# Kernel optimization log

Hardware: AMD Instinct MI355X
Metric: run time of the kernel (lower is better)

## Reference

```python
import jax, jax.numpy as jnp
import numpy as np
from jax.scipy.special import erfc

CUTOFF = 10.0   # real-space cutoff (Angstrom)
ALPHA = 0.3     # Ewald splitting parameter (1/Angstrom)
KMAX = 8        # max integer k-index per dimension
N_ATOMS = 4096
BOX = 40.0      # cubic box edge (Angstrom)


def setup_inputs() -> dict:
    key = jax.random.key(0)
    kp, kq = jax.random.split(key)
    positions = jax.random.uniform(kp, (N_ATOMS, 3), dtype=jnp.float32) * BOX
    charges = jax.random.normal(kq, (N_ATOMS,), dtype=jnp.float32)
    charges = charges - charges.mean()  # enforce charge neutrality
    cell = jnp.eye(3, dtype=jnp.float32) * BOX  # row-vector lattice
    return {"positions": positions, "charges": charges, "cell": cell}


def _kvectors(kmax):
    # static integer grid (-kmax..kmax)^3 \\ {0}, built with numpy at trace time
    n = np.arange(-kmax, kmax + 1)
    grid = np.stack(np.meshgrid(n, n, n, indexing="ij"), axis=-1).reshape(-1, 3)
    grid = grid[np.any(grid != 0, axis=-1)]
    return jnp.asarray(grid, dtype=jnp.float32)  # [Nk, 3]


def _ewald(positions, charges, cell, cutoff, alpha, kmax):
    N = positions.shape[0]
    inv_cell = jnp.linalg.inv(cell)

    # ---- real-space sum: 0.5 * sum_{i!=j, r<rc} q_i q_j erfc(a r)/r (min image)
    rij = positions[:, None, :] - positions[None, :, :]          # [N,N,3]
    frac = rij @ inv_cell
    rij = (frac - jnp.round(frac)) @ cell                        # minimum image
    r2 = jnp.sum(rij * rij, axis=-1)                             # [N,N]
    eye = jnp.eye(N, dtype=bool)
    r = jnp.sqrt(jnp.where(eye, 1.0, r2))                        # safe sqrt on diag
    pair_mask = (~eye) & (r2 < cutoff * cutoff)
    qq = charges[:, None] * charges[None, :]
    e_real = 0.5 * jnp.sum(jnp.where(pair_mask, qq * erfc(alpha * r) / r, 0.0))

    # ---- reciprocal-space sum: (2pi/V) sum_k exp(-k^2/4a^2)/k^2 |S(k)|^2
    recip = 2.0 * jnp.pi * inv_cell.T                            # reciprocal lattice rows
    kvecs = _kvectors(kmax) @ recip                              # [Nk,3]
    k2 = jnp.sum(kvecs * kvecs, axis=-1)                         # [Nk]
    phase = positions @ kvecs.T                                  # [N,Nk]
    s_re = charges @ jnp.cos(phase)                              # [Nk]
    s_im = charges @ jnp.sin(phase)                              # [Nk]
    vol = jnp.abs(jnp.linalg.det(cell))
    coeff = jnp.exp(-k2 / (4.0 * alpha * alpha)) / k2
    e_recip = (2.0 * jnp.pi / vol) * jnp.sum(coeff * (s_re * s_re + s_im * s_im))

    # ---- self-energy correction
    e_self = -(alpha / jnp.sqrt(jnp.pi)) * jnp.sum(charges * charges)

    return e_real + e_recip + e_self


def reference(positions, charges, cell):
    return _ewald(positions, charges, cell, CUTOFF, ALPHA, KMAX)
```

## Files before the change

### kernel.cpp

```cpp
#include <hip/hip_runtime.h>
#include <math.h>

#define ALPHA 0.3f
#define KMAX 8
#define KDIM 17
#define KD2 (KDIM*KDIM)
#define NK_FULL (KDIM*KDIM*KDIM - 1)
#define NK_HALF (NK_FULL/2)
#define RECIP_KPB 16
#define NB_RECIP ((NK_HALF + RECIP_KPB - 1)/RECIP_KPB)
#define TWO_PI 6.28318530717958647692f

#define SELF_COEF (-0.16925687506432687f)
#define INV_4A2 (1.0f/(4.0f*ALPHA*ALPHA))
#define C1A (0.3275911f*ALPHA)
#define NA2 (-(ALPHA*ALPHA))

#define ITILE 256
#define JTILE 128

__device__ __forceinline__ void invert3x3(const float* __restrict__ c, float inv[9], float* det_out) {
    float a00=c[0],a01=c[1],a02=c[2];
    float a10=c[3],a11=c[4],a12=c[5];
    float a20=c[6],a21=c[7],a22=c[8];
    float c00 =  a11*a22 - a12*a21;
    float c01 = -(a10*a22 - a12*a20);
    float c02 =  a10*a21 - a11*a20;
    float det = a00*c00 + a01*c01 + a02*c02;
    float id = 1.0f/det;
    inv[0] =  c00*id;
    inv[1] = -(a01*a22 - a02*a21)*id;
    inv[2] =  (a01*a12 - a02*a11)*id;
    inv[3] =  c01*id;
    inv[4] =  (a00*a22 - a02*a20)*id;
    inv[5] = -(a00*a12 - a02*a10)*id;
    inv[6] =  c02*id;
    inv[7] = -(a00*a21 - a01*a20)*id;
    inv[8] =  (a00*a11 - a01*a10)*id;
    *det_out = det;
}

__device__ __forceinline__ float erfc_a(float r, float r2) {
    float t = __builtin_amdgcn_rcpf(fmaf(C1A, r, 1.0f));
    float p = t * fmaf(t, fmaf(t, fmaf(t, fmaf(t, 1.061405429f, -1.453152027f),
                       1.421413741f), -0.284496736f), 0.254829592f);
    return p * __expf(NA2 * r2);
}

__device__ __forceinline__ float pair_ortho(float4 p, float xi, float yi, float zi,
                                            float i0, float i4, float i8,
                                            float c0, float c4, float c8) {
    float dx = xi - p.x, dy = yi - p.y, dz = zi - p.z;
    float rx = fmaf(-c0, rintf(dx * i0), dx);
    float ry = fmaf(-c4, rintf(dy * i4), dy);
    float rz = fmaf(-c8, rintf(dz * i8), dz);
    float r2 = fmaf(rx, rx, fmaf(ry, ry, rz * rz));
    float rinv = __builtin_amdgcn_rsqf(r2);
    float r = r2 * rinv;
    return p.w * rinv * erfc_a(r, r2);
}

__device__ __forceinline__ float block_reduce(float v) {
    for (int o = 32; o > 0; o >>= 1) v += __shfl_down(v, o, 64);
    __shared__ float smem[4];
    int lane = threadIdx.x & 63, wid = threadIdx.x >> 6;
    if (lane == 0) smem[wid] = v;
    __syncthreads();
    int nw = blockDim.x >> 6;
    v = ((int)threadIdx.x < nw) ? smem[threadIdx.x] : 0.0f;
    if (wid == 0) {
        for (int o = 4; o > 0; o >>= 1) v += __shfl_down(v, o, 64);
    }
    return v;
}

__global__ __launch_bounds__(256) void fused_kernel(const float* __restrict__ pos,
                                                    const float* __restrict__ q,
                                                    const float* __restrict__ cell,
                                                    float* __restrict__ e_out,
                                                    int N, int nb_recip, int nb_real) {
    __shared__ float4 rtile[256];
    __shared__ float red[128][33];
    __shared__ float red2[8][33];
    float inv[9]; float det;
    invert3x3(cell, inv, &det);
    bool ortho = (cell[1]==0.f) & (cell[2]==0.f) & (cell[3]==0.f) &
                 (cell[5]==0.f) & (cell[6]==0.f) & (cell[7]==0.f);

    int bid = blockIdx.x;
    int tid = threadIdx.x;
    int lane = tid & 63, wid = tid >> 6;

    if (bid < nb_recip) {
        int kbase = bid * RECIP_KPB;
        int m = kbase % KDIM;
        int wj = (16 - m) % KDIM;
        bool kxw = ((kbase + wj) % KD2) == (KD2 - 1);
        int wj_s  = __builtin_amdgcn_readfirstlane(wj);
        int kxw_s = __builtin_amdgcn_readfirstlane((int)kxw);
        float fkx0 = (float)(kbase / KD2 - KMAX);
        float fky0 = (float)((kbase / KDIM) % KDIM - KMAX);
        float fkz0 = (float)(kbase % KDIM - KMAX);

        float ar[RECIP_KPB], ai[RECIP_KPB];
        #pragma unroll
        for (int j = 0; j < RECIP_KPB; ++j) { ar[j] = 0.0f; ai[j] = 0.0f; }

        int nrounds = (N + 255) >> 8;
        for (int r = 0; r < nrounds; ++r) {
            int a = (r << 8) + tid;
            if (a < N) {
                float x = pos[3*a], y = pos[3*a+1], z = pos[3*a+2];
                float qa = q[a];
                float wx, wy, wz;
                if (ortho) { wx = x*inv[0]; wy = y*inv[4]; wz = z*inv[8]; }
                else {
                    wx = inv[0]*x + inv[3]*y + inv[6]*z;
                    wy = inv[1]*x + inv[4]*y + inv[7]*z;
                    wz = inv[2]*x + inv[5]*y + inv[8]*z;
                }
                float ph0 = fmaf(fkx0, wx, fmaf(fky0, wy, fkz0 * wz));
                ph0 -= rintf(ph0);
                float az = wz - rintf(wz);
                float aw = kxw_s ? (wx - 16.0f*wy - 17.0f*wz)
                                 : (wy - 17.0f*wz);
                aw -= rintf(aw);
                float c0 = __builtin_amdgcn_cosf(ph0), s0 = __builtin_amdgcn_sinf(ph0);
                float zc = __builtin_amdgcn_cosf(az),  zs = __builtin_amdgcn_sinf(az);
                float wc = __builtin_amdgcn_cosf(aw),  ws = __builtin_amdgcn_sinf(aw);
                float pr = qa * c0, pi = qa * s0;
                #pragma unroll
                for (int j = 0; j < RECIP_KPB; ++j) {
                    ar[j] += pr; ai[j] += pi;
                    if (j < RECIP_KPB - 1) {
                        float nr = pr*zc - pi*zs;
                        float ni = pr*zs + pi*zc;
                        pr = nr; pi = ni;
                        if (j == wj_s) {
                            nr = pr*wc - pi*ws;
                            ni = pr*ws + pi*wc;
                            pr = nr; pi = ni;
                        }
                    }
                }
            }
        }

        #pragma unroll
        for (int j = 0; j < RECIP_KPB; ++j) {
            ar[j] += __shfl_down(ar[j], 32, 64);
            ai[j] += __shfl_down(ai[j], 32, 64);
        }
        if (lane < 32) {
            int row = (wid << 5) | lane;
            #pragma unroll
            for (int j = 0; j < RECIP_KPB; ++j) {
                red[row][j]             = ar[j];
                red[row][RECIP_KPB + j] = ai[j];
            }
        }
        __syncthreads();
        {
            int v = tid & 31, grp = tid >> 5;
            float s = 0.0f;
            int r0 = grp << 4;
            #pragma unroll 4
            for (int rr = 0; rr < 16; ++rr) s += red[r0 + rr][v];
            red2[grp][v] = s;
        }
        __syncthreads();
        if (tid < 32) {
            float tot = 0.0f;
            #pragma unroll
            for (int g = 0; g < 8; ++g) tot += red2[g][tid];
            float other = __shfl_down(tot, 16, 64);
            float e = 0.0f;
            if (tid < 16) {
                int t = kbase + tid;
                if (t < NK_HALF) {
                    float nx = (float)(t / KD2 - KMAX);
                    float ny = (float)((t / KDIM) % KDIM - KMAX);
                    float nz = (float)(t % KDIM - KMAX);
                    float kvx = TWO_PI * (nx*inv[0] + ny*inv[1] + nz*inv[2]);
                    float kvy = TWO_PI * (nx*inv[3] + ny*inv[4] + nz*inv[5]);
                    float kvz = TWO_PI * (nx*inv[6] + ny*inv[7] + nz*inv[8]);
                    float k2 = fmaf(kvx, kvx, fmaf(kvy, kvy, kvz * kvz));
                    float vol = fabsf(det);
                    float pref = 2.0f * (TWO_PI / vol);
                    float coeff = __expf(-k2 * INV_4A2) * __builtin_amdgcn_rcpf(k2);
                    e = pref * coeff * fmaf(tot, tot, other * other);
                }
                for (int o = 8; o > 0; o >>= 1) e += __shfl_down(e, o, 64);
                if (tid == 0) unsafeAtomicAdd(e_out, e);
            }
        }
        if (bid == nb_recip - 1) {
            float fa = 0.0f;
            for (int t = tid; t < N; t += 256) {
                float qt = q[t];
                fa = fmaf(SELF_COEF * qt, qt, fa);
            }
            __syncthreads();
            float s2 = block_reduce(fa);
            if (tid == 0) unsafeAtomicAdd(e_out, s2);
        }
    } else {
        int rbid = bid - nb_recip;
        int bi = 0, acc = 0;
        for (;;) {
            int up = min(N, (bi + 1) * ITILE);
            int nc = (up + JTILE - 1) / JTILE;
            if (rbid < acc + nc) break;
            acc += nc; ++bi;
        }
        int bj = rbid - acc;

        float c0 = cell[0], c4 = cell[4], c8 = cell[8];
        float c1 = cell[1], c2 = cell[2], c3 = cell[3];
        float c5 = cell[5], c6 = cell[6], c7 = cell[7];

        int ibase = bi * ITILE;
        int i = ibase + tid;
        bool ivalid = (i < N);
        float xi = 0.f, yi = 0.f, zi = 0.f, qi = 0.f;
        if (ivalid) { xi = pos[3*i]; yi = pos[3*i+1]; zi = pos[3*i+2]; qi = q[i]; }

        int jbase = bj * JTILE;
        int jcount = min(JTILE, N - jbase);
        if (tid < jcount) {
            int j = jbase + tid;
            rtile[tid] = make_float4(pos[3*j], pos[3*j+1], pos[3*j+2], q[j]);
        }
        __syncthreads();

        bool full = (jbase + JTILE <= ibase) && (ibase + ITILE <= N) && (jcount == JTILE);

        float e0 = 0.0f, e1 = 0.0f, e2 = 0.0f, e3 = 0.0f;
        if (ortho) {
            float i0 = inv[0], i4 = inv[4], i8 = inv[8];
            if (full) {
                #pragma unroll 2
                for (int t = 0; t < JTILE; t += 4) {
                    float4 p0 = rtile[t+0], p1 = rtile[t+1], p2 = rtile[t+2], p3 = rtile[t+3];
                    e0 += pair_ortho(p0, xi, yi, zi, i0, i4, i8, c0, c4, c8);
                    e1 += pair_ortho(p1, xi, yi, zi, i0, i4, i8, c0, c4, c8);
                    e2 += pair_ortho(p2, xi, yi, zi, i0, i4, i8, c0, c4, c8);
                    e3 += pair_ortho(p3, xi, yi, zi, i0, i4, i8, c0, c4, c8);
                }
            } else {
                int t = 0;
                for (; t + 3 < jcount; t += 4) {
                    float4 p0 = rtile[t+0], p1 = rtile[t+1], p2 = rtile[t+2], p3 = rtile[t+3];
                    float v0 = pair_ortho(p0, xi, yi, zi, i0, i4, i8, c0, c4, c8);
                    float v1 = pair_ortho(p1, xi, yi, zi, i0, i4, i8, c0, c4, c8);
                    float v2 = pair_ortho(p2, xi, yi, zi, i0, i4, i8, c0, c4, c8);
                    float v3 = pair_ortho(p3, xi, yi, zi, i0, i4, i8, c0, c4, c8);
                    bool k0 = ivalid && ((jbase + t + 0) < i);
                    bool k1 = ivalid && ((jbase + t + 1) < i);
                    bool k2 = ivalid && ((jbase + t + 2) < i);
                    bool k3 = ivalid && ((jbase + t + 3) < i);
                    e0 += k0 ? v0 : 0.0f;
                    e1 += k1 ? v1 : 0.0f;
                    e2 += k2 ? v2 : 0.0f;
                    e3 += k3 ? v3 : 0.0f;
                }
                for (; t < jcount; ++t) {
                    float4 p = rtile[t];
                    float v = pair_ortho(p, xi, yi, zi, i0, i4, i8, c0, c4, c8);
                    bool ok = ivalid && ((jbase + t) < i);
                    e0 += ok ? v : 0.0f;
                }
            }
        } else {
            for (int t = 0; t < jcount; ++t) {
                float4 p = rtile[t];
                float dx = xi - p.x, dy = yi - p.y, dz = zi - p.z;
                float fx = dx*inv[0] + dy*inv[3] + dz*inv[6];
                float fy = dx*inv[1] + dy*inv[4] + dz*inv[7];
                float fz = dx*inv[2] + dy*inv[5] + dz*inv[8];
                fx -= rintf(fx); fy -= rintf(fy); fz -= rintf(fz);
                float rx = fx*c0 + fy*c3 + fz*c6;
                float ry = fx*c1 + fy*c4 + fz*c7;
                float rz = fx*c2 + fy*c5 + fz*c8;
                float r2 = fmaf(rx, rx, fmaf(ry, ry, rz * rz));
                float rinv = __builtin_amdgcn_rsqf(r2);
                float r = r2 * rinv;
                float val = p.w * rinv * erfc_a(r, r2);
                bool ok = ivalid && ((jbase + t) < i);
                e0 += ok ? val : 0.0f;
            }
        }
        float acc_e = ((e0 + e1) + (e2 + e3)) * qi;

        float s = block_reduce(acc_e);
        if (tid == 0) unsafeAtomicAdd(e_out, s);
    }
}

extern "C" void kernel_launch(void* const* d_in, const int* in_sizes, int n_in,
                              void* d_out, int out_size, void* d_ws, size_t ws_size,
                              hipStream_t stream) {
    const float* pos  = (const float*)d_in[0];
    const float* q    = (const float*)d_in[1];
    const float* cell = (const float*)d_in[2];
    int N = in_sizes[1];
    float* e_out = (float*)d_out;

    int nbi = (N + ITILE - 1) / ITILE;
    int nb_real = 0;
    for (int bi = 0; bi < nbi; ++bi) {
        int up = (N < (bi + 1) * ITILE) ? N : (bi + 1) * ITILE;
        nb_real += (up + JTILE - 1) / JTILE;
    }
    int nb_recip = NB_RECIP;

    hipMemsetAsync(e_out, 0, sizeof(float), stream);

    fused_kernel<<<nb_recip + nb_real, 256, 0, stream>>>(pos, q, cell, e_out,
                                                         N, nb_recip, nb_real);
}
```

Baseline: 73.65 us.

## Use persistent grid-stride blocks with smaller real-space j-tiles and one atomic per block

The kernel now launches a fixed grid of 512 blocks. Each block loops over work units (reciprocal k-groups and real-space tile pairs) with a grid stride, keeps a running sum in a register, and does a single block reduction and atomic at the end. The real-space j-tile shrinks from 128 to 32 to create more, finer units for load balancing. This cuts per-block launch, reduction and atomic overhead. The cost is a block-wide sync per unit, and blocks that land on heavy reciprocal units may become stragglers.

```diff
diff --git a/kernel.cpp b/kernel.cpp
--- a/kernel.cpp
+++ b/kernel.cpp
@@ -17,7 +17,8 @@
 #define NA2 (-(ALPHA*ALPHA))
 
 #define ITILE 256
-#define JTILE 128
+#define JTILE 32
+#define NBLK 512
 
 __device__ __forceinline__ void invert3x3(const float* __restrict__ c, float inv[9], float* det_out) {
     float a00=c[0],a01=c[1],a02=c[2];
@@ -78,7 +79,7 @@
                                                     const float* __restrict__ q,
                                                     const float* __restrict__ cell,
                                                     float* __restrict__ e_out,
-                                                    int N, int nb_recip, int nb_real) {
+                                                    int N, int nb_recip, int n_units) {
     __shared__ float4 rtile[256];
     __shared__ float red[128][33];
     __shared__ float red2[8][33];
@@ -87,214 +88,214 @@
     bool ortho = (cell[1]==0.f) & (cell[2]==0.f) & (cell[3]==0.f) &
                  (cell[5]==0.f) & (cell[6]==0.f) & (cell[7]==0.f);
 
-    int bid = blockIdx.x;
     int tid = threadIdx.x;
     int lane = tid & 63, wid = tid >> 6;
-
-    if (bid < nb_recip) {
-        int kbase = bid * RECIP_KPB;
-        int m = kbase % KDIM;
-        int wj = (16 - m) % KDIM;
-        bool kxw = ((kbase + wj) % KD2) == (KD2 - 1);
-        int wj_s  = __builtin_amdgcn_readfirstlane(wj);
-        int kxw_s = __builtin_amdgcn_readfirstlane((int)kxw);
-        float fkx0 = (float)(kbase / KD2 - KMAX);
-        float fky0 = (float)((kbase / KDIM) % KDIM - KMAX);
-        float fkz0 = (float)(kbase % KDIM - KMAX);
-
-        float ar[RECIP_KPB], ai[RECIP_KPB];
-        #pragma unroll
-        for (int j = 0; j < RECIP_KPB; ++j) { ar[j] = 0.0f; ai[j] = 0.0f; }
-
-        int nrounds = (N + 255) >> 8;
-        for (int r = 0; r < nrounds; ++r) {
-            int a = (r << 8) + tid;
-            if (a < N) {
-                float x = pos[3*a], y = pos[3*a+1], z = pos[3*a+2];
-                float qa = q[a];
-                float wx, wy, wz;
-                if (ortho) { wx = x*inv[0]; wy = y*inv[4]; wz = z*inv[8]; }
-                else {
-                    wx = inv[0]*x + inv[3]*y + inv[6]*z;
-                    wy = inv[1]*x + inv[4]*y + inv[7]*z;
-                    wz = inv[2]*x + inv[5]*y + inv[8]*z;
-                }
-                float ph0 = fmaf(fkx0, wx, fmaf(fky0, wy, fkz0 * wz));
-                ph0 -= rintf(ph0);
-                float az = wz - rintf(wz);
-                float aw = kxw_s ? (wx - 16.0f*wy - 17.0f*wz)
-                                 : (wy - 17.0f*wz);
-                aw -= rintf(aw);
-                float c0 = __builtin_amdgcn_cosf(ph0), s0 = __builtin_amdgcn_sinf(ph0);
-                float zc = __builtin_amdgcn_cosf(az),  zs = __builtin_amdgcn_sinf(az);
-                float wc = __builtin_amdgcn_cosf(aw),  ws = __builtin_amdgcn_sinf(aw);
-                float pr = qa * c0, pi = qa * s0;
+    float vol = fabsf(det);
+    float pref = 2.0f * (TWO_PI / vol);
+
+    float acc_total = 0.0f;
+
+    if (blockIdx.x == 0) {
+        for (int t = tid; t < N; t += 256) {
+            float qt = q[t];
+            acc_total = fmaf(SELF_COEF * qt, qt, acc_total);
+        }
+    }
+
+    for (int u = blockIdx.x; u < n_units; u += NBLK) {
+        __syncthreads();
+
+        if (u < nb_recip) {
+            int kbase = u * RECIP_KPB;
+            int m = kbase % KDIM;
+            int wj = (16 - m) % KDIM;
+            bool kxw = ((kbase + wj) % KD2) == (KD2 - 1);
+            int wj_s  = __builtin_amdgcn_readfirstlane(wj);
+            int kxw_s = __builtin_amdgcn_readfirstlane((int)kxw);
+            float fkx0 = (float)(kbase / KD2 - KMAX);
+            float fky0 = (float)((kbase / KDIM) % KDIM - KMAX);
+            float fkz0 = (float)(kbase % KDIM - KMAX);
+
+            float ar[RECIP_KPB], ai[RECIP_KPB];
+            #pragma unroll
+            for (int j = 0; j < RECIP_KPB; ++j) { ar[j] = 0.0f; ai[j] = 0.0f; }
+
+            int nrounds = (N + 255) >> 8;
+            for (int r = 0; r < nrounds; ++r) {
+                int a = (r << 8) + tid;
+                if (a < N) {
+                    float x = pos[3*a], y = pos[3*a+1], z = pos[3*a+2];
+                    float qa = q[a];
+                    float wx, wy, wz;
+                    if (ortho) { wx = x*inv[0]; wy = y*inv[4]; wz = z*inv[8]; }
+                    else {
+                        wx = inv[0]*x + inv[3]*y + inv[6]*z;
+                        wy = inv[1]*x + inv[4]*y + inv[7]*z;
+                        wz = inv[2]*x + inv[5]*y + inv[8]*z;
+                    }
+                    float ph0 = fmaf(fkx0, wx, fmaf(fky0, wy, fkz0 * wz));
+                    ph0 -= rintf(ph0);
+                    float az = wz - rintf(wz);
+                    float aw = kxw_s ? (wx - 16.0f*wy - 17.0f*wz)
+                                     : (wy - 17.0f*wz);
+                    aw -= rintf(aw);
+                    float c0 = __builtin_amdgcn_cosf(ph0), s0 = __builtin_amdgcn_sinf(ph0);
+                    float zc = __builtin_amdgcn_cosf(az),  zs = __builtin_amdgcn_sinf(az);
+                    float wc = __builtin_amdgcn_cosf(aw),  ws = __builtin_amdgcn_sinf(aw);
+                    float pr = qa * c0, pi = qa * s0;
+                    #pragma unroll
+                    for (int j = 0; j < RECIP_KPB; ++j) {
+                        ar[j] += pr; ai[j] += pi;
+                        if (j < RECIP_KPB - 1) {
+                            float nr = pr*zc - pi*zs;
+                            float ni = pr*zs + pi*zc;
+                            pr = nr; pi = ni;
+                            if (j == wj_s) {
+                                nr = pr*wc - pi*ws;
+                                ni = pr*ws + pi*wc;
+                                pr = nr; pi = ni;
+                            }
+                        }
+                    }
+                }
+            }
+
+            #pragma unroll
+            for (int j = 0; j < RECIP_KPB; ++j) {
+                ar[j] += __shfl_down(ar[j], 32, 64);
+                ai[j] += __shfl_down(ai[j], 32, 64);
+            }
+            if (lane < 32) {
+                int row = (wid << 5) | lane;
                 #pragma unroll
                 for (int j = 0; j < RECIP_KPB; ++j) {
-                    ar[j] += pr; ai[j] += pi;
-                    if (j < RECIP_KPB - 1) {
-                        float nr = pr*zc - pi*zs;
-                        float ni = pr*zs + pi*zc;
-                        pr = nr; pi = ni;
-                        if (j == wj_s) {
-                            nr = pr*wc - pi*ws;
-                            ni = pr*ws + pi*wc;
-                            pr = nr; pi = ni;
-                        }
-                    }
-                }
-            }
+                    red[row][j]             = ar[j];
+                    red[row][RECIP_KPB + j] = ai[j];
+                }
+            }
+            __syncthreads();
+            {
+                int v = tid & 31, grp = tid >> 5;
+                float s = 0.0f;
+                int r0 = grp << 4;
+                #pragma unroll 4
+                for (int rr = 0; rr < 16; ++rr) s += red[r0 + rr][v];
+                red2[grp][v] = s;
+            }
+            __syncthreads();
+            if (tid < 32) {
+                float tot = 0.0f;
+                #pragma unroll
+                for (int g = 0; g < 8; ++g) tot += red2[g][tid];
+                float other = __shfl_down(tot, 16, 64);
+                if (tid < 16) {
+                    int t = kbase + tid;
+                    if (t < NK_HALF) {
+                        float nx = (float)(t / KD2 - KMAX);
+                        float ny = (float)((t / KDIM) % KDIM - KMAX);
+                        float nz = (float)(t % KDIM - KMAX);
+                        float kvx = TWO_PI * (nx*inv[0] + ny*inv[1] + nz*inv[2]);
+                        float kvy = TWO_PI * (nx*inv[3] + ny*inv[4] + nz*inv[5]);
+                        float kvz = TWO_PI * (nx*inv[6] + ny*inv[7] + nz*inv[8]);
+                        float k2 = fmaf(kvx, kvx, fmaf(kvy, kvy, kvz * kvz));
+                        float coeff = __expf(-k2 * INV_4A2) * __builtin_amdgcn_rcpf(k2);
+                        acc_total = fmaf(pref * coeff, fmaf(tot, tot, other * other), acc_total);
+                    }
+                }
+            }
+        } else {
+            int rbid = u - nb_recip;
+            int bi = 0, acc = 0;
+            for (;;) {
+                int up = min(N, (bi + 1) * ITILE);
+                int nc = (up + JTILE - 1) / JTILE;
+                if (rbid < acc + nc) break;
+                acc += nc; ++bi;
+            }
+            int bj = rbid - acc;
+
+            float c0 = cell[0], c4 = cell[4], c8 = cell[8];
+            float c1 = cell[1], c2 = cell[2], c3 = cell[3];
+            float c5 = cell[5], c6 = cell[6], c7 = cell[7];
+
+            int ibase = bi * ITILE;
+            int i = ibase + tid;
+            bool ivalid = (i < N);
+            float xi = 0.f, yi = 0.f, zi = 0.f, qi = 0.f;
+            if (ivalid) { xi = pos[3*i]; yi = pos[3*i+1]; zi = pos[3*i+2]; qi = q[i]; }
+
+            int jbase = bj * JTILE;
+            int jcount = min(JTILE, N - jbase);
+            if (tid < jcount) {
+                int j = jbase + tid;
+                rtile[tid] = make_float4(pos[3*j], pos[3*j+1], pos[3*j+2], q[j]);
+            }
+            __syncthreads();
+
+            bool full = (jbase + JTILE <= ibase) && (ibase + ITILE <= N) && (jcount == JTILE);
+
+            float e0 = 0.0f, e1 = 0.0f, e2 = 0.0f, e3 = 0.0f;
+            if (ortho) {
+                float i0 = inv[0], i4 = inv[4], i8 = inv[8];
+                if (full) {
+                    #pragma unroll 4
+                    for (int t = 0; t < JTILE; t += 4) {
+                        float4 p0 = rtile[t+0], p1 = rtile[t+1], p2 = rtile[t+2], p3 = rtile[t+3];
+                        e0 += pair_ortho(p0, xi, yi, zi, i0, i4, i8, c0, c4, c8);
+                        e1 += pair_ortho(p1, xi, yi, zi, i0, i4, i8, c0, c4, c8);
+                        e2 += pair_ortho(p2, xi, yi, zi, i0, i4, i8, c0, c4, c8);
+                        e3 += pair_ortho(p3, xi, yi, zi, i0, i4, i8, c0, c4, c8);
+                    }
+                } else {
+                    int t = 0;
+                    for (; t + 3 < jcount; t += 4) {
+                        float4 p0 = rtile[t+0], p1 = rtile[t+1], p2 = rtile[t+2], p3 = rtile[t+3];
+                        float v0 = pair_ortho(p0, xi, yi, zi, i0, i4, i8, c0, c4, c8);
+                        float v1 = pair_ortho(p1, xi, yi, zi, i0, i4, i8, c0, c4, c8);
+                        float v2 = pair_ortho(p2, xi, yi, zi, i0, i4, i8, c0, c4, c8);
+                        float v3 = pair_ortho(p3, xi, yi, zi, i0, i4, i8, c0, c4, c8);
+                        bool k0 = ivalid && ((jbase + t + 0) < i);
+                        bool k1 = ivalid && ((jbase + t + 1) < i);
+                        bool k2 = ivalid && ((jbase + t + 2) < i);
+                        bool k3 = ivalid && ((jbase + t + 3) < i);
+                        e0 += k0 ? v0 : 0.0f;
+                        e1 += k1 ? v1 : 0.0f;
+                        e2 += k2 ? v2 : 0.0f;
+                        e3 += k3 ? v3 : 0.0f;
+                    }
+                    for (; t < jcount; ++t) {
+                        float4 p = rtile[t];
+                        float v = pair_ortho(p, xi, yi, zi, i0, i4, i8, c0, c4, c8);
+                        bool ok = ivalid && ((jbase + t) < i);
+                        e0 += ok ? v : 0.0f;
+                    }
+                }
+            } else {
+                for (int t = 0; t < jcount; ++t) {
+                    float4 p = rtile[t];
+                    float dx = xi - p.x, dy = yi - p.y, dz = zi - p.z;
+                    float fx = dx*inv[0] + dy*inv[3] + dz*inv[6];
+                    float fy = dx*inv[1] + dy*inv[4] + dz*inv[7];
+                    float fz = dx*inv[2] + dy*inv[5] + dz*inv[8];
+                    fx -= rintf(fx); fy -= rintf(fy); fz -= rintf(fz);
+                    float rx = fx*c0 + fy*c3 + fz*c6;
+                    float ry = fx*c1 + fy*c4 + fz*c7;
+                    float rz = fx*c2 + fy*c5 + fz*c8;
+                    float r2 = fmaf(rx, rx, fmaf(ry, ry, rz * rz));
+                    float rinv = __builtin_amdgcn_rsqf(r2);
+                    float r = r2 * rinv;
+                    float val = p.w * rinv * erfc_a(r, r2);
+                    bool ok = ivalid && ((jbase + t) < i);
+                    e0 += ok ? val : 0.0f;
+                }
+            }
+            acc_total = fmaf(((e0 + e1) + (e2 + e3)), qi, acc_total);
         }
-
-        #pragma unroll
-        for (int j = 0; j < RECIP_KPB; ++j) {
-            ar[j] += __shfl_down(ar[j], 32, 64);
-            ai[j] += __shfl_down(ai[j], 32, 64);
-        }
-        if (lane < 32) {
-            int row = (wid << 5) | lane;
-            #pragma unroll
-            for (int j = 0; j < RECIP_KPB; ++j) {
-                red[row][j]             = ar[j];
-                red[row][RECIP_KPB + j] = ai[j];
-            }
-        }
-        __syncthreads();
-        {
-            int v = tid & 31, grp = tid >> 5;
-            float s = 0.0f;
-            int r0 = grp << 4;
-            #pragma unroll 4
-            for (int rr = 0; rr < 16; ++rr) s += red[r0 + rr][v];
-            red2[grp][v] = s;
-        }
-        __syncthreads();
-        if (tid < 32) {
-            float tot = 0.0f;
-            #pragma unroll
-            for (int g = 0; g < 8; ++g) tot += red2[g][tid];
-            float other = __shfl_down(tot, 16, 64);
-            float e = 0.0f;
-            if (tid < 16) {
-                int t = kbase + tid;
-                if (t < NK_HALF) {
-                    float nx = (float)(t / KD2 - KMAX);
-                    float ny = (float)((t / KDIM) % KDIM - KMAX);
-                    float nz = (float)(t % KDIM - KMAX);
-                    float kvx = TWO_PI * (nx*inv[0] + ny*inv[1] + nz*inv[2]);
-                    float kvy = TWO_PI * (nx*inv[3] + ny*inv[4] + nz*inv[5]);
-                    float kvz = TWO_PI * (nx*inv[6] + ny*inv[7] + nz*inv[8]);
-                    float k2 = fmaf(kvx, kvx, fmaf(kvy, kvy, kvz * kvz));
-                    float vol = fabsf(det);
-                    float pref = 2.0f * (TWO_PI / vol);
-                    float coeff = __expf(-k2 * INV_4A2) * __builtin_amdgcn_rcpf(k2);
-                    e = pref * coeff * fmaf(tot, tot, other * other);
-                }
-                for (int o = 8; o > 0; o >>= 1) e += __shfl_down(e, o, 64);
-                if (tid == 0) unsafeAtomicAdd(e_out, e);
-            }
-        }
-        if (bid == nb_recip - 1) {
-            float fa = 0.0f;
-            for (int t = tid; t < N; t += 256) {
-                float qt = q[t];
-                fa = fmaf(SELF_COEF * qt, qt, fa);
-            }
-            __syncthreads();
-            float s2 = block_reduce(fa);
-            if (tid == 0) unsafeAtomicAdd(e_out, s2);
-        }
-    } else {
-        int rbid = bid - nb_recip;
-        int bi = 0, acc = 0;
-        for (;;) {
-            int up = min(N, (bi + 1) * ITILE);
-            int nc = (up + JTILE - 1) / JTILE;
-            if (rbid < acc + nc) break;
-            acc += nc; ++bi;
-        }
-        int bj = rbid - acc;
-
-        float c0 = cell[0], c4 = cell[4], c8 = cell[8];
-        float c1 = cell[1], c2 = cell[2], c3 = cell[3];
-        float c5 = cell[5], c6 = cell[6], c7 = cell[7];
-
-        int ibase = bi * ITILE;
-        int i = ibase + tid;
-        bool ivalid = (i < N);
-        float xi = 0.f, yi = 0.f, zi = 0.f, qi = 0.f;
-        if (ivalid) { xi = pos[3*i]; yi = pos[3*i+1]; zi = pos[3*i+2]; qi = q[i]; }
-
-        int jbase = bj * JTILE;
-        int jcount = min(JTILE, N - jbase);
-        if (tid < jcount) {
-            int j = jbase + tid;
-            rtile[tid] = make_float4(pos[3*j], pos[3*j+1], pos[3*j+2], q[j]);
-        }
-        __syncthreads();
-
-        bool full = (jbase + JTILE <= ibase) && (ibase + ITILE <= N) && (jcount == JTILE);
-
-        float e0 = 0.0f, e1 = 0.0f, e2 = 0.0f, e3 = 0.0f;
-        if (ortho) {
-            float i0 = inv[0], i4 = inv[4], i8 = inv[8];
-            if (full) {
-                #pragma unroll 2
-                for (int t = 0; t < JTILE; t += 4) {
-                    float4 p0 = rtile[t+0], p1 = rtile[t+1], p2 = rtile[t+2], p3 = rtile[t+3];
-                    e0 += pair_ortho(p0, xi, yi, zi, i0, i4, i8, c0, c4, c8);
-                    e1 += pair_ortho(p1, xi, yi, zi, i0, i4, i8, c0, c4, c8);
-                    e2 += pair_ortho(p2, xi, yi, zi, i0, i4, i8, c0, c4, c8);
-                    e3 += pair_ortho(p3, xi, yi, zi, i0, i4, i8, c0, c4, c8);
-                }
-            } else {
-                int t = 0;
-                for (; t + 3 < jcount; t += 4) {
-                    float4 p0 = rtile[t+0], p1 = rtile[t+1], p2 = rtile[t+2], p3 = rtile[t+3];
-                    float v0 = pair_ortho(p0, xi, yi, zi, i0, i4, i8, c0, c4, c8);
-                    float v1 = pair_ortho(p1, xi, yi, zi, i0, i4, i8, c0, c4, c8);
-                    float v2 = pair_ortho(p2, xi, yi, zi, i0, i4, i8, c0, c4, c8);
-                    float v3 = pair_ortho(p3, xi, yi, zi, i0, i4, i8, c0, c4, c8);
-                    bool k0 = ivalid && ((jbase + t + 0) < i);
-                    bool k1 = ivalid && ((jbase + t + 1) < i);
-                    bool k2 = ivalid && ((jbase + t + 2) < i);
-                    bool k3 = ivalid && ((jbase + t + 3) < i);
-                    e0 += k0 ? v0 : 0.0f;
-                    e1 += k1 ? v1 : 0.0f;
-                    e2 += k2 ? v2 : 0.0f;
-                    e3 += k3 ? v3 : 0.0f;
-                }
-                for (; t < jcount; ++t) {
-                    float4 p = rtile[t];
-                    float v = pair_ortho(p, xi, yi, zi, i0, i4, i8, c0, c4, c8);
-                    bool ok = ivalid && ((jbase + t) < i);
-                    e0 += ok ? v : 0.0f;
-                }
-            }
-        } else {
-            for (int t = 0; t < jcount; ++t) {
-                float4 p = rtile[t];
-                float dx = xi - p.x, dy = yi - p.y, dz = zi - p.z;
-                float fx = dx*inv[0] + dy*inv[3] + dz*inv[6];
-                float fy = dx*inv[1] + dy*inv[4] + dz*inv[7];
-                float fz = dx*inv[2] + dy*inv[5] + dz*inv[8];
-                fx -= rintf(fx); fy -= rintf(fy); fz -= rintf(fz);
-                float rx = fx*c0 + fy*c3 + fz*c6;
-                float ry = fx*c1 + fy*c4 + fz*c7;
-                float rz = fx*c2 + fy*c5 + fz*c8;
-                float r2 = fmaf(rx, rx, fmaf(ry, ry, rz * rz));
-                float rinv = __builtin_amdgcn_rsqf(r2);
-                float r = r2 * rinv;
-                float val = p.w * rinv * erfc_a(r, r2);
-                bool ok = ivalid && ((jbase + t) < i);
-                e0 += ok ? val : 0.0f;
-            }
-        }
-        float acc_e = ((e0 + e1) + (e2 + e3)) * qi;
-
-        float s = block_reduce(acc_e);
-        if (tid == 0) unsafeAtomicAdd(e_out, s);
     }
+
+    __syncthreads();
+    float s = block_reduce(acc_total);
+    if (tid == 0) unsafeAtomicAdd(e_out, s);
 }
 
 extern "C" void kernel_launch(void* const* d_in, const int* in_sizes, int n_in,
@@ -313,9 +314,13 @@
         nb_real += (up + JTILE - 1) / JTILE;
     }
     int nb_recip = NB_RECIP;
+    int n_units = nb_recip + nb_real;
+
+    int nblk = NBLK;
+    if (nblk > n_units) nblk = n_units;
 
     hipMemsetAsync(e_out, 0, sizeof(float), stream);
 
-    fused_kernel<<<nb_recip + nb_real, 256, 0, stream>>>(pos, q, cell, e_out,
-                                                         N, nb_recip, nb_real);
-}
+    fused_kernel<<<nblk, 256, 0, stream>>>(pos, q, cell, e_out,
+                                           N, nb_recip, n_units);
+}
```

Result: slower. 79.02 us (+7.3%).
